# Kernel tuning notes

Hardware: AMD Instinct MI355X
Metric: run time of the kernel (lower is better)

Reference implementation:

```python
import jax, jax.numpy as jnp
import numpy as np

# Fixed average-trace buffer from the module (length 120)
AVG = jnp.asarray([0.0256,0.0823,0.1157,0.1315,0.1366,0.1369,0.1347,0.1308,0.1259,0.1205,0.1146,0.1086,0.1028,0.097,0.0913,0.0858,0.0805,0.0756,0.0708,0.0664,0.0623,0.0584,0.0549,0.0515,0.0485,0.0456,0.0429,0.0404,0.0381,0.036,0.034,0.0321,0.0304,0.0287,0.0272,0.0258,0.0245,0.0233,0.0222,0.0211,0.0201,0.0191,0.0182,0.0173,0.0165,0.0158,0.015,0.0143,0.0137,0.013,0.0125,0.0119,0.0114,0.0108,0.0104,0.0099,0.0095,0.0091,0.0087,0.0083,0.008,0.0077,0.0074,0.0071,0.0068,0.0065,0.0062,0.006,0.0058,0.0055,0.0053,0.005,0.0049,0.0047,0.0045,0.0044,0.0042,0.004,0.0039,0.0038,0.0036,0.0034,0.0033,0.0032,0.0031,0.003,0.0029,0.0028,0.0027,0.0026,0.0025,0.0024,0.0023,0.0022,0.0021,0.0021,0.002,0.0019,0.0018,0.0018,0.0017,0.0017,0.0016,0.0016,0.0015,0.0015,0.0014,0.0014,0.0013,0.0013,0.0013,0.0012,0.0012,0.0011,0.0011,0.0011,0.001,0.001,0.001,0.0009], dtype=jnp.float32)


def _lstm(x, w_ih, w_hh, b):
    """PyTorch-semantics single-layer LSTM. x: [N,T,D], w_ih: [4H,D], w_hh: [4H,H], b: [4H] (= b_ih + b_hh). Gate order i,f,g,o."""
    xp = jnp.einsum('ntd,gd->ntg', x, w_ih) + b  # precompute input projections: [N,T,4H]
    N = x.shape[0]
    H = w_hh.shape[1]
    h0 = jnp.zeros((N, H), x.dtype)

    def step(carry, xt):
        h, c = carry
        g = xt + h @ w_hh.T  # [N,4H]
        i, f, gg, o = jnp.split(g, 4, axis=-1)
        c = jax.nn.sigmoid(f) * c + jax.nn.sigmoid(i) * jnp.tanh(gg)
        h = jax.nn.sigmoid(o) * jnp.tanh(c)
        return (h, c), h

    _, hs = jax.lax.scan(step, (h0, h0), jnp.swapaxes(xp, 0, 1))  # hs: [T,N,H]
    return jnp.swapaxes(hs, 0, 1)  # [N,T,H]


def setup_inputs() -> dict:
    key = jax.random.key(0)
    ks = jax.random.split(key, 7)
    N, F, H = 32768, 12, 30
    s1 = 1.0 / float(np.sqrt(H))  # torch LSTM init: U(-1/sqrt(H), 1/sqrt(H))
    s2 = 1.0                      # second LSTM hidden=1 -> scale 1
    return {
        'features': jax.random.normal(ks[0], (N, F), jnp.float32),
        'w_ih1': jax.random.uniform(ks[1], (4 * H, F + 1), jnp.float32, -s1, s1),
        'w_hh1': jax.random.uniform(ks[2], (4 * H, H), jnp.float32, -s1, s1),
        'b1': jax.random.uniform(ks[3], (4 * H,), jnp.float32, -s1, s1),
        'w_ih2': jax.random.uniform(ks[4], (4, H), jnp.float32, -s2, s2),
        'w_hh2': jax.random.uniform(ks[5], (4, 1), jnp.float32, -s2, s2),
        'b2': jax.random.uniform(ks[6], (4,), jnp.float32, -s2, s2),
    }


def reference(features, w_ih1, w_hh1, b1, w_ih2, w_hh2, b2):
    N, F = features.shape
    T = AVG.shape[0]  # 120
    x = jnp.broadcast_to(features[:, None, :], (N, T, F))          # repeat features over time
    trace = jnp.broadcast_to(AVG[None, :, None], (N, T, 1))        # average trace channel
    x = jnp.concatenate([x, trace], axis=2)                        # [N,120,13]
    h1 = _lstm(x, w_ih1, w_hh1, b1)                                # [N,120,30]
    return _lstm(h1, w_ih2, w_hh2, b2)                             # [N,120,1]
```

## Files before the change

kernel.cpp:

```cpp
#include <hip/hip_runtime.h>

typedef __attribute__((ext_vector_type(8))) short bf16x8;
typedef __attribute__((ext_vector_type(4))) float f32x4;

#define LOG2E 1.44269504088896340736f

__device__ __constant__ float AVG_D[120] = {
    0.0256f,0.0823f,0.1157f,0.1315f,0.1366f,0.1369f,0.1347f,0.1308f,0.1259f,0.1205f,
    0.1146f,0.1086f,0.1028f,0.0970f,0.0913f,0.0858f,0.0805f,0.0756f,0.0708f,0.0664f,
    0.0623f,0.0584f,0.0549f,0.0515f,0.0485f,0.0456f,0.0429f,0.0404f,0.0381f,0.0360f,
    0.0340f,0.0321f,0.0304f,0.0287f,0.0272f,0.0258f,0.0245f,0.0233f,0.0222f,0.0211f,
    0.0201f,0.0191f,0.0182f,0.0173f,0.0165f,0.0158f,0.0150f,0.0143f,0.0137f,0.0130f,
    0.0125f,0.0119f,0.0114f,0.0108f,0.0104f,0.0099f,0.0095f,0.0091f,0.0087f,0.0083f,
    0.0080f,0.0077f,0.0074f,0.0071f,0.0068f,0.0065f,0.0062f,0.0060f,0.0058f,0.0055f,
    0.0053f,0.0050f,0.0049f,0.0047f,0.0045f,0.0044f,0.0042f,0.0040f,0.0039f,0.0038f,
    0.0036f,0.0034f,0.0033f,0.0032f,0.0031f,0.0030f,0.0029f,0.0028f,0.0027f,0.0026f,
    0.0025f,0.0024f,0.0023f,0.0022f,0.0021f,0.0021f,0.0020f,0.0019f,0.0018f,0.0018f,
    0.0017f,0.0017f,0.0016f,0.0016f,0.0015f,0.0015f,0.0014f,0.0014f,0.0013f,0.0013f,
    0.0013f,0.0012f,0.0012f,0.0011f,0.0011f,0.0011f,0.0010f,0.0010f,0.0010f,0.0009f
};

__device__ __forceinline__ float sig2(float x) {
    return __builtin_amdgcn_rcpf(1.0f + __builtin_amdgcn_exp2f(x));
}
__device__ __forceinline__ float tanh2(float x) {
    return fmaf(2.0f, __builtin_amdgcn_rcpf(1.0f + __builtin_amdgcn_exp2f(x)), -1.0f);
}
__device__ __forceinline__ unsigned short tb(float x) {
    return (unsigned short)(__float_as_uint(x) >> 16);
}
__device__ __forceinline__ float fb(unsigned short h) {
    return __uint_as_float(((unsigned)h) << 16);
}

__global__ void pack_weights(const float* __restrict__ w_ih1,
                             const float* __restrict__ w_hh1,
                             const float* __restrict__ b1,
                             const float* __restrict__ w_ih2,
                             const float* __restrict__ b2,
                             float* __restrict__ ws) {
    unsigned short* whi = (unsigned short*)ws;
    unsigned short* wlo = (unsigned short*)(ws + 2048);
    float* bconst = ws + 4096;
    float* wih1f  = ws + 4224;
    unsigned* avgpk = (unsigned*)(ws + 5760);
    const int tid = threadIdx.x;
    for (int idx = tid; idx < 4096; idx += 256) {
        const int T = idx >> 9, lane = (idx >> 3) & 63, j = idx & 7;
        const int r = 16 * T + (lane & 15);
        const int k = ((lane >> 4) & 3) * 8 + j;
        const int u = r >> 2, q = r & 3;
        const float sc = (q == 2) ? (-2.0f * LOG2E) : (-LOG2E);
        float v = 0.0f;
        if (u < 30) {
            if (k < 30)       v = w_hh1[(q * 30 + u) * 30 + k];
            else if (k == 30) v = w_ih1[(q * 30 + u) * 13 + 12];
        } else if (u == 30 && k < 30) {
            v = w_ih2[q * 30 + k];
        }
        v *= sc;
        const unsigned short hi = tb(v);
        whi[idx] = hi;
        wlo[idx] = tb(v - fb(hi));
    }
    for (int r = tid; r < 128; r += 256) {
        const int u = r >> 2, q = r & 3;
        const float sc = (q == 2) ? (-2.0f * LOG2E) : (-LOG2E);
        bconst[r] = sc * ((u < 30) ? b1[q * 30 + u] : ((u == 30) ? b2[q] : 0.0f));
    }
    for (int idx = tid; idx < 1536; idx += 256) {
        const int r = idx / 12, d = idx % 12;
        const int u = r >> 2, q = r & 3;
        const float sc = (q == 2) ? (-2.0f * LOG2E) : (-LOG2E);
        wih1f[idx] = (u < 30) ? sc * w_ih1[(q * 30 + u) * 13 + d] : 0.0f;
    }
    for (int t = tid; t < 121; t += 256) {
        const float a = (t < 120) ? AVG_D[t] : 0.0f;
        const unsigned short hi = tb(a);
        const unsigned short lo = tb(a - fb(hi));
        avgpk[t] = (unsigned)hi | ((unsigned)lo << 16);
    }
}

__global__ __launch_bounds__(128, 4)
void lstm_mfma_kernel(const float* __restrict__ feat,
                      const float* __restrict__ w_hh2,
                      const float* __restrict__ ws,
                      float* __restrict__ out) {
    __shared__ __align__(16) unsigned hx[2][16 * 36];
    __shared__ __align__(16) float out_s[16 * 124];

    const int tid  = threadIdx.x;
    const int lane = tid & 63;
    const int wv   = __builtin_amdgcn_readfirstlane(tid >> 6);
    const int s    = lane & 15;
    const int quad = lane >> 4;
    const int seq  = blockIdx.x * 16 + s;
    const unsigned* avgpk = (const unsigned*)(ws + 5760);

    for (int i = tid; i < 2 * 16 * 36; i += 128) (&hx[0][0])[i] = 0u;
    __syncthreads();
    if (tid < 16) hx[0][tid * 36 + 30] = avgpk[0];

    bf16x8 Ahi[4], Alo[4];
    {
        const unsigned short* whi = (const unsigned short*)ws;
        const unsigned short* wlo = (const unsigned short*)(ws + 2048);
#pragma unroll
        for (int T = 0; T < 4; T++) {
            const int Tg = 4 * wv + T;
            Ahi[T] = *(const bf16x8*)(whi + Tg * 512 + lane * 8);
            Alo[T] = *(const bf16x8*)(wlo + Tg * 512 + lane * 8);
        }
    }

    float f0[12];
    {
        const float4* fp = reinterpret_cast<const float4*>(feat + seq * 12);
        float4 A = fp[0], B = fp[1], C = fp[2];
        f0[0]=A.x; f0[1]=A.y; f0[2]=A.z; f0[3]=A.w;
        f0[4]=B.x; f0[5]=B.y; f0[6]=B.z; f0[7]=B.w;
        f0[8]=C.x; f0[9]=C.y; f0[10]=C.z; f0[11]=C.w;
    }
    f32x4 projb[4];
    {
        const float* bconst = ws + 4096;
        const float* wih1f  = ws + 4224;
#pragma unroll
        for (int T = 0; T < 4; T++) {
#pragma unroll
            for (int g = 0; g < 4; g++) {
                const int r = 16 * (4 * wv + T) + 4 * quad + g;
                float acc = bconst[r];
#pragma unroll
                for (int d = 0; d < 12; d++) acc = fmaf(f0[d], wih1f[r * 12 + d], acc);
                projb[T][g] = acc;
            }
        }
    }

    float c1[4];
#pragma unroll
    for (int T = 0; T < 4; T++) c1[T] = 0.0f;
    float h2 = 0.0f, c2 = 0.0f;
    const float whs0 = -LOG2E * w_hh2[0];
    const float whs1 = -LOG2E * w_hh2[1];
    const float whs2 = -2.0f * LOG2E * w_hh2[2];
    const float whs3 = -LOG2E * w_hh2[3];

    __syncthreads();

    unsigned apk_cur = avgpk[1];

#pragma unroll 1
    for (int t = 0; t <= 120; t++) {
        const unsigned* hb = hx[t & 1];
        unsigned*       hn = hx[(t & 1) ^ 1];

        const unsigned apk = apk_cur;
        apk_cur = avgpk[(t + 2 <= 120) ? (t + 2) : 120];

        const uint4 Ra = *reinterpret_cast<const uint4*>(hb + s * 36 + 8 * quad);
        const uint4 Rb = *reinterpret_cast<const uint4*>(hb + s * 36 + 8 * quad + 4);
        union { int4 i; bf16x8 v; } ubh, ubl;
        ubh.i.x = (int)__builtin_amdgcn_perm(Ra.y, Ra.x, 0x05040100u);
        ubh.i.y = (int)__builtin_amdgcn_perm(Ra.w, Ra.z, 0x05040100u);
        ubh.i.z = (int)__builtin_amdgcn_perm(Rb.y, Rb.x, 0x05040100u);
        ubh.i.w = (int)__builtin_amdgcn_perm(Rb.w, Rb.z, 0x05040100u);
        ubl.i.x = (int)__builtin_amdgcn_perm(Ra.y, Ra.x, 0x07060302u);
        ubl.i.y = (int)__builtin_amdgcn_perm(Ra.w, Ra.z, 0x07060302u);
        ubl.i.z = (int)__builtin_amdgcn_perm(Rb.y, Rb.x, 0x07060302u);
        ubl.i.w = (int)__builtin_amdgcn_perm(Rb.w, Rb.z, 0x07060302u);
        const bf16x8 Bhi = ubh.v, Blo = ubl.v;

        f32x4 D[4];
#pragma unroll
        for (int T = 0; T < 4; T++)
            D[T] = __builtin_amdgcn_mfma_f32_16x16x32_bf16(Alo[T], Bhi, projb[T], 0, 0, 0);
#pragma unroll
        for (int T = 0; T < 4; T++)
            D[T] = __builtin_amdgcn_mfma_f32_16x16x32_bf16(Ahi[T], Blo, D[T], 0, 0, 0);
#pragma unroll
        for (int T = 0; T < 4; T++)
            D[T] = __builtin_amdgcn_mfma_f32_16x16x32_bf16(Ahi[T], Bhi, D[T], 0, 0, 0);

        if (wv == 1 && t >= 1 && quad == 2) {
            const float g0 = fmaf(h2, whs0, D[3][0]);
            const float g1 = fmaf(h2, whs1, D[3][1]);
            const float g2 = fmaf(h2, whs2, D[3][2]);
            const float g3 = fmaf(h2, whs3, D[3][3]);
            c2 = sig2(g1) * c2 + sig2(g0) * tanh2(g2);
            h2 = sig2(g3) * tanh2(c2 * (-2.0f * LOG2E));
            out_s[s * 124 + (t - 1)] = h2;
        }

        if (t < 120) {
#pragma unroll
            for (int T = 0; T < 4; T++) {
                const int u = 16 * wv + 4 * T + quad;
                unsigned v = 0u;
                if (u < 30) {
                    const float ei = __builtin_amdgcn_exp2f(D[T][0]);
                    const float ef = __builtin_amdgcn_exp2f(D[T][1]);
                    const float eg = __builtin_amdgcn_exp2f(D[T][2]);
                    const float eo = __builtin_amdgcn_exp2f(D[T][3]);
                    const float pi_ = 1.0f + ei, pf = 1.0f + ef;
                    const float pg  = 1.0f + eg, po = 1.0f + eo;
                    const float pig = pi_ * pg;
                    const float num = fmaf(c1[T], pig, (1.0f - eg) * pf);
                    const float ck  = num * __builtin_amdgcn_rcpf(pf * pig);
                    c1[T] = ck;
                    float carg = -2.0f * LOG2E * ck;
                    carg = fminf(fmaxf(carg, -80.0f), 80.0f);
                    const float ec = __builtin_amdgcn_exp2f(carg);
                    const float hk = (1.0f - ec) *
                                     __builtin_amdgcn_rcpf(po * (1.0f + ec));
                    const unsigned hbits = __float_as_uint(hk);
                    const float rem = hk - __uint_as_float(hbits & 0xffff0000u);
                    v = __builtin_amdgcn_perm(__float_as_uint(rem), hbits, 0x07060302u);
                } else if (u == 30) {
                    v = apk;
                }
                hn[s * 36 + u] = v;
            }
            __syncthreads();
        }
    }

    __syncthreads();
    float* outb = out + (size_t)blockIdx.x * 16 * 120;
#pragma unroll
    for (int it = 0; it < 4; it++) {
        const int fi = it * 128 + tid;
        if (fi < 480) {
            const int sq = fi / 30, j = fi % 30;
            const float4 v = *reinterpret_cast<const float4*>(&out_s[sq * 124 + j * 4]);
            *reinterpret_cast<float4*>(&outb[sq * 120 + j * 4]) = v;
        }
    }
}

extern "C" void kernel_launch(void* const* d_in, const int* in_sizes, int n_in,
                              void* d_out, int out_size, void* d_ws, size_t ws_size,
                              hipStream_t stream) {
    (void)in_sizes; (void)n_in; (void)out_size; (void)ws_size;
    const float* feat  = (const float*)d_in[0];
    const float* w_ih1 = (const float*)d_in[1];
    const float* w_hh1 = (const float*)d_in[2];
    const float* b1    = (const float*)d_in[3];
    const float* w_ih2 = (const float*)d_in[4];
    const float* w_hh2 = (const float*)d_in[5];
    const float* b2    = (const float*)d_in[6];
    float* ws  = (float*)d_ws;
    float* out = (float*)d_out;

    hipLaunchKernelGGL(pack_weights, dim3(1), dim3(256), 0, stream,
                       w_ih1, w_hh1, b1, w_ih2, b2, ws);
    hipLaunchKernelGGL(lstm_mfma_kernel, dim3(2048), dim3(128), 0, stream,
                       feat, w_hh2, ws, out);
}
```

Baseline: 257.3 us.

## Split hidden-state LDS into hi/lo bf16 planes and batch reciprocals

Stores the recurrent hidden state as two separate bf16 planes (hi and lo) in shared memory, so the MFMA B operands load directly as bf16x8 vectors and the per-step byte-permute unpacking goes away. The gate math now runs branch-free for all four tiles. Pairs of reciprocals are merged into one rcp via the product trick, and the tanh clamp range is narrowed. The cost is 16-bit scattered LDS stores (two per element instead of one 32-bit store) and some extra work on padded units.

```diff
diff --git a/kernel.cpp b/kernel.cpp
--- a/kernel.cpp
+++ b/kernel.cpp
@@ -87,30 +87,39 @@
                       const float* __restrict__ w_hh2,
                       const float* __restrict__ ws,
                       float* __restrict__ out) {
-    __shared__ __align__(16) unsigned hx[2][16 * 36];
+    __shared__ __align__(16) unsigned short hhi[2][16 * 40];
+    __shared__ __align__(16) unsigned short hlo[2][16 * 40];
     __shared__ __align__(16) float out_s[16 * 124];
 
     const int tid  = threadIdx.x;
     const int lane = tid & 63;
-    const int wv   = __builtin_amdgcn_readfirstlane(tid >> 6);
+    const int wv   = __builtin_amdgcn_readfirstlane(tid >> 6) & 1;
     const int s    = lane & 15;
     const int quad = lane >> 4;
     const int seq  = blockIdx.x * 16 + s;
     const unsigned* avgpk = (const unsigned*)(ws + 5760);
 
-    for (int i = tid; i < 2 * 16 * 36; i += 128) (&hx[0][0])[i] = 0u;
+    {
+        unsigned* zh = (unsigned*)(&hhi[0][0]);
+        unsigned* zl = (unsigned*)(&hlo[0][0]);
+        for (int i = tid; i < 640; i += 128) { zh[i] = 0u; zl[i] = 0u; }
+    }
     __syncthreads();
-    if (tid < 16) hx[0][tid * 36 + 30] = avgpk[0];
+    if (tid < 16) {
+        const unsigned a0 = avgpk[0];
+        hhi[0][tid * 40 + 30] = (unsigned short)a0;
+        hlo[0][tid * 40 + 30] = (unsigned short)(a0 >> 16);
+    }
 
     bf16x8 Ahi[4], Alo[4];
     {
-        const unsigned short* whi = (const unsigned short*)ws;
-        const unsigned short* wlo = (const unsigned short*)(ws + 2048);
+        const unsigned short* wahi = (const unsigned short*)ws;
+        const unsigned short* walo = (const unsigned short*)(ws + 2048);
 #pragma unroll
         for (int T = 0; T < 4; T++) {
             const int Tg = 4 * wv + T;
-            Ahi[T] = *(const bf16x8*)(whi + Tg * 512 + lane * 8);
-            Alo[T] = *(const bf16x8*)(wlo + Tg * 512 + lane * 8);
+            Ahi[T] = *(const bf16x8*)(wahi + Tg * 512 + lane * 8);
+            Alo[T] = *(const bf16x8*)(walo + Tg * 512 + lane * 8);
         }
     }
 
@@ -154,24 +163,17 @@
 
 #pragma unroll 1
     for (int t = 0; t <= 120; t++) {
-        const unsigned* hb = hx[t & 1];
-        unsigned*       hn = hx[(t & 1) ^ 1];
+        const int buf = t & 1;
+        const unsigned short* bh = hhi[buf];
+        const unsigned short* bl = hlo[buf];
+        unsigned short* nh = hhi[buf ^ 1];
+        unsigned short* nl = hlo[buf ^ 1];
 
         const unsigned apk = apk_cur;
         apk_cur = avgpk[(t + 2 <= 120) ? (t + 2) : 120];
 
-        const uint4 Ra = *reinterpret_cast<const uint4*>(hb + s * 36 + 8 * quad);
-        const uint4 Rb = *reinterpret_cast<const uint4*>(hb + s * 36 + 8 * quad + 4);
-        union { int4 i; bf16x8 v; } ubh, ubl;
-        ubh.i.x = (int)__builtin_amdgcn_perm(Ra.y, Ra.x, 0x05040100u);
-        ubh.i.y = (int)__builtin_amdgcn_perm(Ra.w, Ra.z, 0x05040100u);
-        ubh.i.z = (int)__builtin_amdgcn_perm(Rb.y, Rb.x, 0x05040100u);
-        ubh.i.w = (int)__builtin_amdgcn_perm(Rb.w, Rb.z, 0x05040100u);
-        ubl.i.x = (int)__builtin_amdgcn_perm(Ra.y, Ra.x, 0x07060302u);
-        ubl.i.y = (int)__builtin_amdgcn_perm(Ra.w, Ra.z, 0x07060302u);
-        ubl.i.z = (int)__builtin_amdgcn_perm(Rb.y, Rb.x, 0x07060302u);
-        ubl.i.w = (int)__builtin_amdgcn_perm(Rb.w, Rb.z, 0x07060302u);
-        const bf16x8 Bhi = ubh.v, Blo = ubl.v;
+        const bf16x8 Bhi = *(const bf16x8*)(bh + s * 40 + 8 * quad);
+        const bf16x8 Blo = *(const bf16x8*)(bl + s * 40 + 8 * quad);
 
         f32x4 D[4];
 #pragma unroll
@@ -195,33 +197,48 @@
         }
 
         if (t < 120) {
+            float s2a[4], Ba[4], hka[4];
+#pragma unroll
+            for (int T = 0; T < 4; T++) {
+                const float ei = __builtin_amdgcn_exp2f(D[T][0]);
+                const float ef = __builtin_amdgcn_exp2f(D[T][1]);
+                const float eg = __builtin_amdgcn_exp2f(D[T][2]);
+                const float eo = __builtin_amdgcn_exp2f(D[T][3]);
+                const float pi_ = 1.0f + ei, pf = 1.0f + ef;
+                const float pg  = 1.0f + eg, po = 1.0f + eo;
+                const float pig = pi_ * pg;
+                const float num = fmaf(c1[T], pig, (1.0f - eg) * pf);
+                const float ck  = num * __builtin_amdgcn_rcpf(pf * pig);
+                c1[T] = ck;
+                float carg = -2.0f * LOG2E * ck;
+                carg = fminf(fmaxf(carg, -20.0f), 20.0f);
+                const float ec = __builtin_amdgcn_exp2f(carg);
+                s2a[T] = 1.0f - ec;
+                Ba[T]  = po * (1.0f + ec);
+            }
+            {
+                const float P01 = __builtin_amdgcn_rcpf(Ba[0] * Ba[1]);
+                hka[0] = s2a[0] * (Ba[1] * P01);
+                hka[1] = s2a[1] * (Ba[0] * P01);
+                const int u3 = 16 * wv + 12 + quad;
+                const float B3e = (u3 < 30) ? Ba[3] : 1.0f;
+                const float P23 = __builtin_amdgcn_rcpf(Ba[2] * B3e);
+                hka[2] = s2a[2] * (B3e * P23);
+                hka[3] = s2a[3] * (Ba[2] * P23);
+            }
 #pragma unroll
             for (int T = 0; T < 4; T++) {
                 const int u = 16 * wv + 4 * T + quad;
-                unsigned v = 0u;
-                if (u < 30) {
-                    const float ei = __builtin_amdgcn_exp2f(D[T][0]);
-                    const float ef = __builtin_amdgcn_exp2f(D[T][1]);
-                    const float eg = __builtin_amdgcn_exp2f(D[T][2]);
-                    const float eo = __builtin_amdgcn_exp2f(D[T][3]);
-                    const float pi_ = 1.0f + ei, pf = 1.0f + ef;
-                    const float pg  = 1.0f + eg, po = 1.0f + eo;
-                    const float pig = pi_ * pg;
-                    const float num = fmaf(c1[T], pig, (1.0f - eg) * pf);
-                    const float ck  = num * __builtin_amdgcn_rcpf(pf * pig);
-                    c1[T] = ck;
-                    float carg = -2.0f * LOG2E * ck;
-                    carg = fminf(fmaxf(carg, -80.0f), 80.0f);
-                    const float ec = __builtin_amdgcn_exp2f(carg);
-                    const float hk = (1.0f - ec) *
-                                     __builtin_amdgcn_rcpf(po * (1.0f + ec));
-                    const unsigned hbits = __float_as_uint(hk);
-                    const float rem = hk - __uint_as_float(hbits & 0xffff0000u);
-                    v = __builtin_amdgcn_perm(__float_as_uint(rem), hbits, 0x07060302u);
-                } else if (u == 30) {
-                    v = apk;
+                const unsigned hbits = __float_as_uint(hka[T]);
+                const float rem = hka[T] - __uint_as_float(hbits & 0xffff0000u);
+                unsigned hi16 = hbits >> 16;
+                unsigned lo16 = __float_as_uint(rem) >> 16;
+                if (T == 3) {
+                    if (u == 30) { hi16 = apk & 0xffffu; lo16 = apk >> 16; }
+                    else if (u == 31) { hi16 = 0u; lo16 = 0u; }
                 }
-                hn[s * 36 + u] = v;
+                nh[s * 40 + u] = (unsigned short)hi16;
+                nl[s * 40 + u] = (unsigned short)lo16;
             }
             __syncthreads();
         }
```

Measured after the change: 246.1 us (median of 2 runs). 4.3% less time.
